# Performance work log

Measured on AMD Instinct MI355X. Metric: run time of the kernel, lower is better.

## Reference

```python
import jax, jax.numpy as jnp
import numpy as np

QB = 64  # quantize_size from the source


def _blockwise_quant(y):
    """y: (N, R, C) softmax output. Quantize in 64x64 tiles to int8.
    Returns (q_int8 [N*g1*g2, QB*QB], s, z) matching the torch code."""
    N, R, C = y.shape
    g1, g2 = R // QB, C // QB
    # (N, g1, QB, g2, QB) -> (N, g1, g2, QB, QB) -> (N*g1*g2, QB*QB)
    b = y.reshape(N, g1, QB, g2, QB).transpose(0, 1, 3, 2, 4).reshape(-1, QB * QB)
    mx = jnp.max(b, axis=-1, keepdims=True)
    mn = jnp.min(b, axis=-1, keepdims=True)
    s = (mx - mn) / 255.0
    z = -mn / (s + 1e-10) - 128.0
    q = jnp.round(jnp.clip(b / (s + 1e-10) + z, -128.0, 127.0)).astype(jnp.int8)
    return q, s, z


def reference(x):
    # Forward: plain softmax over dim=-1; the int8 blockwise quantization is the
    # activation saved for backward (returned here so the workload isn't DCE'd).
    out = jax.nn.softmax(x, axis=-1)
    y = out.reshape(-1, x.shape[-2], x.shape[-1])
    q, s, z = _blockwise_quant(y)
    return out, q, s, z


def setup_inputs():
    key = jax.random.key(0)
    x = jax.random.normal(key, (2, 16, 2048, 2048), dtype=jnp.float32)
    return {"x": x}
```

## Files before the change

kernel.cpp:

```cpp
#include <hip/hip_runtime.h>
#include <math.h>


static constexpr int  COLS      = 2048;
static constexpr long long OUT_ELEMS = 134217728LL;
static constexpr int  NBLK      = 32768;

using v4f = __attribute__((ext_vector_type(4))) float;

__global__ __launch_bounds__(1024) void fused_kernel(
    const float* __restrict__ x,
    float* __restrict__ out, float* __restrict__ qout,
    float* __restrict__ sout, float* __restrict__ zout)
{
    const int b = blockIdx.x;
    const int n = b >> 5;
    const int i = b & 31;
    const int t = threadIdx.x;
    const int w = t >> 6;
    const int l = t & 63;

    const long long xbase = (long long)n * (COLS * (long long)COLS)
                          + (long long)(i * 64) * COLS;

    __shared__ float2 sst[64];

#pragma unroll
    for (int rr = 0; rr < 4; ++rr) {
        const int r = w + rr * 16;
        const float* rp = x + xbase + (long long)r * COLS;
        float4 v[8];
#pragma unroll
        for (int c = 0; c < 8; ++c)
            v[c] = *reinterpret_cast<const float4*>(rp + c * 256 + l * 4);

        float m = -INFINITY;
#pragma unroll
        for (int c = 0; c < 8; ++c)
            m = fmaxf(m, fmaxf(fmaxf(v[c].x, v[c].y), fmaxf(v[c].z, v[c].w)));
#pragma unroll
        for (int off = 32; off >= 1; off >>= 1)
            m = fmaxf(m, __shfl_xor(m, off, 64));

        float s = 0.0f;
#pragma unroll
        for (int c = 0; c < 8; ++c)
            s += __expf(v[c].x - m) + __expf(v[c].y - m) +
                 __expf(v[c].z - m) + __expf(v[c].w - m);
#pragma unroll
        for (int off = 32; off >= 1; off >>= 1)
            s += __shfl_xor(s, off, 64);

        if (l == 0) sst[r] = make_float2(m, 1.0f / s);
    }
    __syncthreads();

#pragma unroll
    for (int jj = 0; jj < 2; ++jj) {
        const int j = w + jj * 16;
        const long long tbase = xbase + j * 64;
        const int cl = (l & 15) * 4;
        const int rl = l >> 4;

        float4 p[16];
        float mn = INFINITY, mx = -INFINITY;
#pragma unroll
        for (int k = 0; k < 16; ++k) {
            const int r = rl + 4 * k;
            const float2 st = sst[r];
            const float4 v = *reinterpret_cast<const float4*>(
                x + tbase + (long long)r * COLS + cl);
            float4 pv;
            pv.x = __expf(v.x - st.x) * st.y;
            pv.y = __expf(v.y - st.x) * st.y;
            pv.z = __expf(v.z - st.x) * st.y;
            pv.w = __expf(v.w - st.x) * st.y;
            p[k] = pv;
            mn = fminf(mn, fminf(fminf(pv.x, pv.y), fminf(pv.z, pv.w)));
            mx = fmaxf(mx, fmaxf(fmaxf(pv.x, pv.y), fmaxf(pv.z, pv.w)));
        }
#pragma unroll
        for (int off = 32; off >= 1; off >>= 1) {
            mn = fminf(mn, __shfl_xor(mn, off, 64));
            mx = fmaxf(mx, __shfl_xor(mx, off, 64));
        }

        const float sc  = (mx - mn) / 255.0f;
        const float d   = sc + 1e-10f;
        const float zz  = -mn / d - 128.0f;
        const float rcp = 1.0f / d;
        const int b4 = (n << 10) + (i << 5) + j;
        if (l == 0) { sout[b4] = sc; zout[b4] = zz; }

        float* __restrict__ qb = qout + (long long)b4 * 4096 + cl;
#pragma unroll
        for (int k = 0; k < 16; ++k) {
            const int r = rl + 4 * k;
            const float4 pv = p[k];
            __builtin_nontemporal_store(*(const v4f*)&pv,
                (v4f*)(out + tbase + (long long)r * COLS + cl));
            float4 qv;
            qv.x = roundf(fminf(fmaxf(pv.x * rcp + zz, -128.0f), 127.0f));
            qv.y = roundf(fminf(fmaxf(pv.y * rcp + zz, -128.0f), 127.0f));
            qv.z = roundf(fminf(fmaxf(pv.z * rcp + zz, -128.0f), 127.0f));
            qv.w = roundf(fminf(fmaxf(pv.w * rcp + zz, -128.0f), 127.0f));
            __builtin_nontemporal_store(*(const v4f*)&qv, (v4f*)(qb + r * 64));
        }
    }
}

extern "C" void kernel_launch(void* const* d_in, const int* in_sizes, int n_in,
                              void* d_out, int out_size, void* d_ws, size_t ws_size,
                              hipStream_t stream) {
    const float* x = (const float*)d_in[0];
    float* out  = (float*)d_out;
    float* qout = out + OUT_ELEMS;
    float* sout = qout + OUT_ELEMS;
    float* zout = sout + NBLK;

    fused_kernel<<<1024, 1024, 0, stream>>>(x, out, qout, sout, zout);
}
```

Before: 416.2 us.

## Split fused softmax-quant into chunked stats and quant kernels reading cached output

The single fused kernel read x twice (once for row stats, once per tile for exp and quant). Now the first kernel computes softmax rows once, writes the output with normal stores, and reduces per-tile min/max through shared memory. A second kernel then rereads the freshly written output to quantize it. The work is issued in four chunks so each chunk's output can still sit in L2/MALL when the quant kernel reads it. This drops the second read of x and the recomputed exp, at the cost of extra kernel launches, an extra read of the output, and the loss of nontemporal stores on the softmax output.

```diff
diff --git a/kernel.cpp b/kernel.cpp
--- a/kernel.cpp
+++ b/kernel.cpp
@@ -5,17 +5,20 @@
 static constexpr int  COLS      = 2048;
 static constexpr long long OUT_ELEMS = 134217728LL;
 static constexpr int  NBLK      = 32768;
+static constexpr int  NCHUNK    = 4;
+static constexpr int  STRIPS_PER_CHUNK = 256;
+static constexpr int  PANELS_PER_CHUNK = 2048;
 
 using v4f = __attribute__((ext_vector_type(4))) float;
 
-__global__ __launch_bounds__(1024) void fused_kernel(
-    const float* __restrict__ x,
-    float* __restrict__ out, float* __restrict__ qout,
-    float* __restrict__ sout, float* __restrict__ zout)
+__global__ __launch_bounds__(1024) void softmax_stats_kernel(
+    const float* __restrict__ x, float* __restrict__ out,
+    float* __restrict__ sout, float* __restrict__ zout,
+    float2* __restrict__ szbuf, int chunk)
 {
-    const int b = blockIdx.x;
-    const int n = b >> 5;
-    const int i = b & 31;
+    const int strip = chunk * STRIPS_PER_CHUNK + blockIdx.x;
+    const int n = strip >> 5;
+    const int i = strip & 31;
     const int t = threadIdx.x;
     const int w = t >> 6;
     const int l = t & 63;
@@ -23,12 +26,13 @@
     const long long xbase = (long long)n * (COLS * (long long)COLS)
                           + (long long)(i * 64) * COLS;
 
-    __shared__ float2 sst[64];
+    __shared__ float2 sT[64][32];
 
 #pragma unroll
     for (int rr = 0; rr < 4; ++rr) {
-        const int r = w + rr * 16;
+        const int r = rr * 16 + w;
         const float* rp = x + xbase + (long long)r * COLS;
+
         float4 v[8];
 #pragma unroll
         for (int c = 0; c < 8; ++c)
@@ -50,62 +54,84 @@
 #pragma unroll
         for (int off = 32; off >= 1; off >>= 1)
             s += __shfl_xor(s, off, 64);
+        const float rcp = 1.0f / s;
 
-        if (l == 0) sst[r] = make_float2(m, 1.0f / s);
+        float* op = out + xbase + (long long)r * COLS;
+#pragma unroll
+        for (int c = 0; c < 8; ++c) {
+            float4 pv;
+            pv.x = __expf(v[c].x - m) * rcp;
+            pv.y = __expf(v[c].y - m) * rcp;
+            pv.z = __expf(v[c].z - m) * rcp;
+            pv.w = __expf(v[c].w - m) * rcp;
+            *reinterpret_cast<float4*>(op + c * 256 + l * 4) = pv;
+
+            float tmn = fminf(fminf(pv.x, pv.y), fminf(pv.z, pv.w));
+            float tmx = fmaxf(fmaxf(pv.x, pv.y), fmaxf(pv.z, pv.w));
+#pragma unroll
+            for (int off = 8; off >= 1; off >>= 1) {
+                tmn = fminf(tmn, __shfl_xor(tmn, off, 64));
+                tmx = fmaxf(tmx, __shfl_xor(tmx, off, 64));
+            }
+            if ((l & 15) == 0)
+                sT[r][4 * c + (l >> 4)] = make_float2(tmn, tmx);
+        }
     }
     __syncthreads();
 
 #pragma unroll
     for (int jj = 0; jj < 2; ++jj) {
-        const int j = w + jj * 16;
-        const long long tbase = xbase + j * 64;
-        const int cl = (l & 15) * 4;
-        const int rl = l >> 4;
-
-        float4 p[16];
-        float mn = INFINITY, mx = -INFINITY;
-#pragma unroll
-        for (int k = 0; k < 16; ++k) {
-            const int r = rl + 4 * k;
-            const float2 st = sst[r];
-            const float4 v = *reinterpret_cast<const float4*>(
-                x + tbase + (long long)r * COLS + cl);
-            float4 pv;
-            pv.x = __expf(v.x - st.x) * st.y;
-            pv.y = __expf(v.y - st.x) * st.y;
-            pv.z = __expf(v.z - st.x) * st.y;
-            pv.w = __expf(v.w - st.x) * st.y;
-            p[k] = pv;
-            mn = fminf(mn, fminf(fminf(pv.x, pv.y), fminf(pv.z, pv.w)));
-            mx = fmaxf(mx, fmaxf(fmaxf(pv.x, pv.y), fmaxf(pv.z, pv.w)));
-        }
+        const int j = 2 * w + jj;
+        const float2 vv = sT[l][j];
+        float mn = vv.x, mx = vv.y;
 #pragma unroll
         for (int off = 32; off >= 1; off >>= 1) {
             mn = fminf(mn, __shfl_xor(mn, off, 64));
             mx = fmaxf(mx, __shfl_xor(mx, off, 64));
         }
+        if (l == 0) {
+            const float sc = (mx - mn) / 255.0f;
+            const float d  = sc + 1e-10f;
+            const float zz = -mn / d - 128.0f;
+            const int g = (n << 10) + (i << 5) + j;
+            sout[g] = sc;
+            zout[g] = zz;
+            szbuf[g] = make_float2(zz, 1.0f / d);
+        }
+    }
+}
 
-        const float sc  = (mx - mn) / 255.0f;
-        const float d   = sc + 1e-10f;
-        const float zz  = -mn / d - 128.0f;
-        const float rcp = 1.0f / d;
-        const int b4 = (n << 10) + (i << 5) + j;
-        if (l == 0) { sout[b4] = sc; zout[b4] = zz; }
+__global__ __launch_bounds__(256) void quant_kernel(
+    const float* __restrict__ out, const float2* __restrict__ szbuf,
+    float* __restrict__ qout, int chunk)
+{
+    const int p  = chunk * PANELS_PER_CHUNK + blockIdx.x;
+    const int n  = p >> 8;
+    const int i  = (p >> 3) & 31;
+    const int jg = p & 7;
+    const int t  = threadIdx.x;
+    const int w  = t >> 6;
+    const int l  = t & 63;
 
-        float* __restrict__ qb = qout + (long long)b4 * 4096 + cl;
+    const long long obase = (long long)n * (COLS * (long long)COLS)
+                          + (long long)(i * 64) * COLS + jg * 256;
+    const int tile4 = (n << 10) + (i << 5) + (jg << 2);
+    const float2 sz = szbuf[tile4 + (l >> 4)];
+
+    float* __restrict__ qb = qout + (long long)tile4 * 4096
+                           + (l >> 4) * 4096 + (l & 15) * 4;
+
 #pragma unroll
-        for (int k = 0; k < 16; ++k) {
-            const int r = rl + 4 * k;
-            const float4 pv = p[k];
-            __builtin_nontemporal_store(*(const v4f*)&pv,
-                (v4f*)(out + tbase + (long long)r * COLS + cl));
-            float4 qv;
-            qv.x = roundf(fminf(fmaxf(pv.x * rcp + zz, -128.0f), 127.0f));
-            qv.y = roundf(fminf(fmaxf(pv.y * rcp + zz, -128.0f), 127.0f));
-            qv.z = roundf(fminf(fmaxf(pv.z * rcp + zz, -128.0f), 127.0f));
-            qv.w = roundf(fminf(fmaxf(pv.w * rcp + zz, -128.0f), 127.0f));
-            __builtin_nontemporal_store(*(const v4f*)&qv, (v4f*)(qb + r * 64));
-        }
+    for (int k = 0; k < 16; ++k) {
+        const int r = 4 * k + w;
+        const float4 pv = *reinterpret_cast<const float4*>(
+            out + obase + (long long)r * COLS + l * 4);
+        float4 qv;
+        qv.x = roundf(fminf(fmaxf(pv.x * sz.y + sz.x, -128.0f), 127.0f));
+        qv.y = roundf(fminf(fmaxf(pv.y * sz.y + sz.x, -128.0f), 127.0f));
+        qv.z = roundf(fminf(fmaxf(pv.z * sz.y + sz.x, -128.0f), 127.0f));
+        qv.w = roundf(fminf(fmaxf(pv.w * sz.y + sz.x, -128.0f), 127.0f));
+        __builtin_nontemporal_store(*(const v4f*)&qv, (v4f*)(qb + r * 64));
     }
 }
 
@@ -117,6 +143,12 @@
     float* qout = out + OUT_ELEMS;
     float* sout = qout + OUT_ELEMS;
     float* zout = sout + NBLK;
+    float2* szbuf = (float2*)d_ws;
 
-    fused_kernel<<<1024, 1024, 0, stream>>>(x, out, qout, sout, zout);
+    for (int c = 0; c < NCHUNK; ++c) {
+        softmax_stats_kernel<<<STRIPS_PER_CHUNK, 1024, 0, stream>>>(
+            x, out, sout, zout, szbuf, c);
+        quant_kernel<<<PANELS_PER_CHUNK, 256, 0, stream>>>(
+            out, szbuf, qout, c);
+    }
 }
```

Result: faster. 404.5 us (-2.8%).
